# Kernel tuning notes

Measured on AMD Instinct MI355X. Metric: run time of the kernel, lower is better.

The kernel has to match this reference:

```python
import jax, jax.numpy as jnp
import numpy as np

BZ, PZ, FZ, FI = 8, 8192, 768, 256


def setup_inputs() -> dict:
    key = jax.random.key(0)
    ks = jax.random.split(key, 8)
    x = jax.random.normal(ks[0], (BZ, PZ, FZ), dtype=jnp.float32)
    # valid lengths per bag, in [1, PZ]
    nonpad = jax.random.randint(ks[1], (BZ,), 1, PZ + 1, dtype=jnp.int64)
    s_v = 1.0 / np.sqrt(FZ)
    V_w = jax.random.uniform(ks[2], (FI, FZ), minval=-s_v, maxval=s_v, dtype=jnp.float32)
    V_b = jax.random.uniform(ks[3], (FI,), minval=-s_v, maxval=s_v, dtype=jnp.float32)
    U_w = jax.random.uniform(ks[4], (FI, FZ), minval=-s_v, maxval=s_v, dtype=jnp.float32)
    U_b = jax.random.uniform(ks[5], (FI,), minval=-s_v, maxval=s_v, dtype=jnp.float32)
    s_w = 1.0 / np.sqrt(FI)
    w_w = jax.random.uniform(ks[6], (1, FI), minval=-s_w, maxval=s_w, dtype=jnp.float32)
    w_b = jax.random.uniform(ks[7], (1,), minval=-s_w, maxval=s_w, dtype=jnp.float32)
    return {"x": x, "nonpad": nonpad, "V_w": V_w, "V_b": V_b, "U_w": U_w, "U_b": U_b, "w_w": w_w, "w_b": w_b}


def reference(x, nonpad, V_w, V_b, U_w, U_b, w_w, w_b):
    # gated attention branches: [b, p, fi]
    att_v = jnp.tanh(jnp.einsum("bpf,if->bpi", x, V_w) + V_b)
    att_u = jax.nn.sigmoid(jnp.einsum("bpf,if->bpi", x, U_w) + U_b)
    # attention logits: [b, p]
    att = jnp.einsum("bpi,oi->bpo", att_u * att_v, w_w)[..., 0] + w_b[0]
    # per-sample masked softmax over first nonpad[b] positions, zeros on pad
    mask = jnp.arange(PZ)[None, :] < nonpad[:, None]  # [b, p]
    neg_inf = jnp.finfo(att.dtype).min
    weight = jax.nn.softmax(jnp.where(mask, att, neg_inf), axis=1)
    weight = jnp.where(mask, weight, 0.0)
    return weight[:, None, :]  # [b, 1, p]
```

## Files before the change

### kernel.cpp

```cpp
#include <hip/hip_runtime.h>
#include <hip/hip_bf16.h>
#include <cmath>

#define BZ 8
#define PZ 8192
#define FZ 768
#define FI 256
#define M_TOTAL (BZ * PZ)
#define BM 128
#define BK 64
#define NKT (FZ / BK)
#define NB_TILE (128 * BK)

typedef __bf16 bf16_t;
typedef __bf16 bf16x8 __attribute__((ext_vector_type(8)));
typedef float f32x4 __attribute__((ext_vector_type(4)));

#define AS1 __attribute__((address_space(1)))
#define AS3 __attribute__((address_space(3)))

__global__ void pack_weights(const float* __restrict__ Vw,
                             const float* __restrict__ Uw,
                             bf16_t* __restrict__ Wc) {
    int pr = blockIdx.x;
    int j = pr >> 5, u = (pr >> 4) & 1, r = pr & 15;
    const float* src = (u ? Uw : Vw) + (size_t)(j * 16 + r) * FZ;
    int nb = pr >> 7, prl = pr & 127;
    for (int k = threadIdx.x; k < FZ; k += blockDim.x) {
        int t = k >> 6, slot = (k >> 3) & 7, jj = k & 7;
        Wc[(size_t)(nb * NKT + t) * NB_TILE + prl * 64 + ((slot ^ (prl & 7)) * 8 + jj)]
            = (bf16_t)src[k];
    }
}

__global__ __launch_bounds__(256, 3)
void gemm_gate(const float* __restrict__ x, const bf16_t* __restrict__ Wc,
               const float* __restrict__ Vb, const float* __restrict__ Ub,
               const float* __restrict__ ww, float* __restrict__ part) {
    __shared__ bf16_t As[BM * BK] __attribute__((aligned(16)));
    __shared__ bf16_t Bs[2][128 * BK] __attribute__((aligned(16)));

    const int bid = blockIdx.x;
    const int nb = (bid >> 3) & 3;
    const int mt = (bid & 7) | ((bid >> 5) << 3);
    const int tid = threadIdx.x;
    const int l = tid & 63, wv = tid >> 6;
    const int wm = wv >> 1, wn = wv & 1;
    const int row0 = mt * BM;

    f32x4 acc[4][4] = {};
    float4 abuf[8];
    const bf16_t* WcB = Wc + (size_t)nb * NKT * NB_TILE;

    auto issueA = [&](int t) {
        #pragma unroll
        for (int i = 0; i < 4; ++i) {
            int sidx = tid + i * 256;
            int row = sidx >> 3, sl = sidx & 7;
            const float* gp = x + (size_t)(row0 + row) * FZ + t * BK + sl * 8;
            abuf[2 * i]     = *(const float4*)gp;
            abuf[2 * i + 1] = *(const float4*)(gp + 4);
        }
    };
    auto writeA = [&]() {
        #pragma unroll
        for (int i = 0; i < 4; ++i) {
            int sidx = tid + i * 256;
            int row = sidx >> 3, sl = sidx & 7;
            float4 f0 = abuf[2 * i], f1 = abuf[2 * i + 1];
            bf16x8 v;
            v[0] = (bf16_t)f0.x; v[1] = (bf16_t)f0.y; v[2] = (bf16_t)f0.z; v[3] = (bf16_t)f0.w;
            v[4] = (bf16_t)f1.x; v[5] = (bf16_t)f1.y; v[6] = (bf16_t)f1.z; v[7] = (bf16_t)f1.w;
            *(bf16x8*)&As[row * 64 + (sl ^ (row & 7)) * 8] = v;
        }
    };
    auto issueB = [&](int t, int buf) {
        const bf16_t* src = WcB + (size_t)t * NB_TILE + wv * 2048 + l * 8;
        bf16_t* dst = &Bs[buf][wv * 2048];
        #pragma unroll
        for (int c = 0; c < 4; ++c)
            __builtin_amdgcn_global_load_lds(
                (const AS1 void*)(src + c * 512),
                (AS3 void*)(dst + c * 512), 16, 0, 0);
    };
    auto compute = [&](int buf) {
        #pragma unroll
        for (int kk = 0; kk < 2; ++kk) {
            int sg = kk * 4 + (l >> 4);
            bf16x8 af[4], bfr[4];
            #pragma unroll
            for (int fm = 0; fm < 4; ++fm) {
                int row = wm * 64 + fm * 16 + (l & 15);
                af[fm] = *(const bf16x8*)&As[row * 64 + ((sg ^ (row & 7)) * 8)];
            }
            #pragma unroll
            for (int fn = 0; fn < 4; ++fn) {
                int col = wn * 64 + fn * 16 + (l & 15);
                bfr[fn] = *(const bf16x8*)&Bs[buf][col * 64 + ((sg ^ (col & 7)) * 8)];
            }
            #pragma unroll
            for (int fm = 0; fm < 4; ++fm)
                #pragma unroll
                for (int fn = 0; fn < 4; ++fn)
                    acc[fm][fn] = __builtin_amdgcn_mfma_f32_16x16x32_bf16(
                        af[fm], bfr[fn], acc[fm][fn], 0, 0, 0);
        }
    };

    issueB(0, 0);
    asm volatile("" ::: "memory");
    issueA(0);
    asm volatile("" ::: "memory");
    writeA();
    asm volatile("s_waitcnt vmcnt(0) lgkmcnt(0)" ::: "memory");
    __builtin_amdgcn_s_barrier();

    #pragma unroll
    for (int t = 0; t < NKT; ++t) {
        const int cur = t & 1;
        if (t + 1 < NKT) {
            issueB(t + 1, cur ^ 1);
            asm volatile("" ::: "memory");
            issueA(t + 1);
            asm volatile("" ::: "memory");
        }
        compute(cur);
        if (t + 1 < NKT) {
            __builtin_amdgcn_s_barrier();
            writeA();
            asm volatile("s_waitcnt vmcnt(0) lgkmcnt(0)" ::: "memory");
            __builtin_amdgcn_s_barrier();
        }
    }

    const int c16 = l & 15;
    float vb[2], ub[2], wf[2];
    #pragma unroll
    for (int q = 0; q < 2; ++q) {
        int o = (nb * 4 + wn * 2 + q) * 16 + c16;
        vb[q] = Vb[o]; ub[q] = Ub[o]; wf[q] = ww[o];
    }
    const int slot = nb * 2 + wn;
    #pragma unroll
    for (int fm = 0; fm < 4; ++fm) {
        #pragma unroll
        for (int e = 0; e < 4; ++e) {
            float partial = 0.f;
            #pragma unroll
            for (int q = 0; q < 2; ++q) {
                float zv = acc[fm][2 * q][e] + vb[q];
                float zu = acc[fm][2 * q + 1][e] + ub[q];
                float th = 1.f - 2.f / (__expf(2.f * zv) + 1.f);
                float sg = 1.f / (1.f + __expf(-zu));
                partial += th * sg * wf[q];
            }
            partial += __shfl_xor(partial, 1);
            partial += __shfl_xor(partial, 2);
            partial += __shfl_xor(partial, 4);
            partial += __shfl_xor(partial, 8);
            if (c16 == 0) {
                int r = row0 + wm * 64 + fm * 16 + (l >> 4) * 4 + e;
                part[(size_t)slot * M_TOTAL + r] = partial;
            }
        }
    }
}

__global__ __launch_bounds__(1024)
void softmax_kernel(const float* __restrict__ part, const int* __restrict__ nonpad,
                    float* __restrict__ out) {
    __shared__ float satt[PZ];
    __shared__ float red[16];
    int b = blockIdx.x;
    int np = nonpad[b];
    int tid = threadIdx.x;

    for (int p = tid; p < PZ; p += 1024) {
        float s = 0.f;
        #pragma unroll
        for (int q = 0; q < 8; ++q) s += part[(size_t)q * M_TOTAL + b * PZ + p];
        satt[p] = s;
    }
    __syncthreads();

    float m = -3.4e38f;
    for (int p = tid; p < np; p += 1024) m = fmaxf(m, satt[p]);
    #pragma unroll
    for (int off = 32; off; off >>= 1) m = fmaxf(m, __shfl_xor(m, off));
    if ((tid & 63) == 0) red[tid >> 6] = m;
    __syncthreads();
    m = red[0];
    #pragma unroll
    for (int i = 1; i < 16; ++i) m = fmaxf(m, red[i]);
    __syncthreads();

    float sum = 0.f;
    for (int p = tid; p < np; p += 1024) sum += __expf(satt[p] - m);
    #pragma unroll
    for (int off = 32; off; off >>= 1) sum += __shfl_xor(sum, off);
    if ((tid & 63) == 0) red[tid >> 6] = sum;
    __syncthreads();
    float S = red[0];
    #pragma unroll
    for (int i = 1; i < 16; ++i) S += red[i];
    float inv = 1.f / S;

    for (int p = tid; p < PZ; p += 1024)
        out[b * PZ + p] = (p < np) ? __expf(satt[p] - m) * inv : 0.f;
}

extern "C" void kernel_launch(void* const* d_in, const int* in_sizes, int n_in,
                              void* d_out, int out_size, void* d_ws, size_t ws_size,
                              hipStream_t stream) {
    const float* x    = (const float*)d_in[0];
    const int* nonpad = (const int*)d_in[1];
    const float* V_w  = (const float*)d_in[2];
    const float* V_b  = (const float*)d_in[3];
    const float* U_w  = (const float*)d_in[4];
    const float* U_b  = (const float*)d_in[5];
    const float* w_w  = (const float*)d_in[6];

    bf16_t* Wc  = (bf16_t*)d_ws;
    float* part = (float*)((char*)d_ws + (size_t)512 * FZ * 2);
    float* out  = (float*)d_out;

    pack_weights<<<512, 128, 0, stream>>>(V_w, U_w, Wc);
    gemm_gate<<<2048, 256, 0, stream>>>(x, Wc, V_b, U_b, w_w, part);
    softmax_kernel<<<8, 1024, 0, stream>>>(part, nonpad, out);
}
```

Before: 94.03 us.

## Load A fragments directly from global into registers, bypassing LDS

Each wave now owns 32 rows and all 128 output columns. It loads its x rows straight from global memory into MFMA-layout registers and converts them to bf16 there, which removes the shared-memory A tile, the writeA stage and one barrier per k-step. Only B still goes through double-buffered LDS, and a partial vmcnt wait lets the next A prefetch stay in flight. The cost is that x loads become less coalesced (16 rows, 32-byte segments per lane group), and each B fragment is now reused across only 2 M-fragments. There are also fewer partial slots for the softmax to sum.

```diff
diff --git a/kernel.cpp b/kernel.cpp
--- a/kernel.cpp
+++ b/kernel.cpp
@@ -37,7 +37,6 @@
 void gemm_gate(const float* __restrict__ x, const bf16_t* __restrict__ Wc,
                const float* __restrict__ Vb, const float* __restrict__ Ub,
                const float* __restrict__ ww, float* __restrict__ part) {
-    __shared__ bf16_t As[BM * BK] __attribute__((aligned(16)));
     __shared__ bf16_t Bs[2][128 * BK] __attribute__((aligned(16)));
 
     const int bid = blockIdx.x;
@@ -45,34 +44,23 @@
     const int mt = (bid & 7) | ((bid >> 5) << 3);
     const int tid = threadIdx.x;
     const int l = tid & 63, wv = tid >> 6;
-    const int wm = wv >> 1, wn = wv & 1;
-    const int row0 = mt * BM;
-
-    f32x4 acc[4][4] = {};
+    const int row0 = mt * BM + wv * 32;
+    const int arow = row0 + (l & 15);
+    const float* xbase = x + (size_t)arow * FZ + (l >> 4) * 8;
+
+    f32x4 acc[2][8] = {};
     float4 abuf[8];
     const bf16_t* WcB = Wc + (size_t)nb * NKT * NB_TILE;
 
     auto issueA = [&](int t) {
         #pragma unroll
-        for (int i = 0; i < 4; ++i) {
-            int sidx = tid + i * 256;
-            int row = sidx >> 3, sl = sidx & 7;
-            const float* gp = x + (size_t)(row0 + row) * FZ + t * BK + sl * 8;
-            abuf[2 * i]     = *(const float4*)gp;
-            abuf[2 * i + 1] = *(const float4*)(gp + 4);
-        }
-    };
-    auto writeA = [&]() {
-        #pragma unroll
-        for (int i = 0; i < 4; ++i) {
-            int sidx = tid + i * 256;
-            int row = sidx >> 3, sl = sidx & 7;
-            float4 f0 = abuf[2 * i], f1 = abuf[2 * i + 1];
-            bf16x8 v;
-            v[0] = (bf16_t)f0.x; v[1] = (bf16_t)f0.y; v[2] = (bf16_t)f0.z; v[3] = (bf16_t)f0.w;
-            v[4] = (bf16_t)f1.x; v[5] = (bf16_t)f1.y; v[6] = (bf16_t)f1.z; v[7] = (bf16_t)f1.w;
-            *(bf16x8*)&As[row * 64 + (sl ^ (row & 7)) * 8] = v;
-        }
+        for (int fm = 0; fm < 2; ++fm)
+            #pragma unroll
+            for (int kk = 0; kk < 2; ++kk) {
+                const float* gp = xbase + (size_t)fm * 16 * FZ + t * BK + kk * 32;
+                abuf[fm * 4 + kk * 2]     = *(const float4*)gp;
+                abuf[fm * 4 + kk * 2 + 1] = *(const float4*)(gp + 4);
+            }
     };
     auto issueB = [&](int t, int buf) {
         const bf16_t* src = WcB + (size_t)t * NB_TILE + wv * 2048 + l * 8;
@@ -83,71 +71,67 @@
                 (const AS1 void*)(src + c * 512),
                 (AS3 void*)(dst + c * 512), 16, 0, 0);
     };
-    auto compute = [&](int buf) {
-        #pragma unroll
-        for (int kk = 0; kk < 2; ++kk) {
-            int sg = kk * 4 + (l >> 4);
-            bf16x8 af[4], bfr[4];
-            #pragma unroll
-            for (int fm = 0; fm < 4; ++fm) {
-                int row = wm * 64 + fm * 16 + (l & 15);
-                af[fm] = *(const bf16x8*)&As[row * 64 + ((sg ^ (row & 7)) * 8)];
-            }
-            #pragma unroll
-            for (int fn = 0; fn < 4; ++fn) {
-                int col = wn * 64 + fn * 16 + (l & 15);
-                bfr[fn] = *(const bf16x8*)&Bs[buf][col * 64 + ((sg ^ (col & 7)) * 8)];
-            }
-            #pragma unroll
-            for (int fm = 0; fm < 4; ++fm)
-                #pragma unroll
-                for (int fn = 0; fn < 4; ++fn)
-                    acc[fm][fn] = __builtin_amdgcn_mfma_f32_16x16x32_bf16(
-                        af[fm], bfr[fn], acc[fm][fn], 0, 0, 0);
-        }
-    };
 
     issueB(0, 0);
     asm volatile("" ::: "memory");
     issueA(0);
     asm volatile("" ::: "memory");
-    writeA();
-    asm volatile("s_waitcnt vmcnt(0) lgkmcnt(0)" ::: "memory");
+    asm volatile("s_waitcnt vmcnt(8)" ::: "memory");
     __builtin_amdgcn_s_barrier();
 
     #pragma unroll
     for (int t = 0; t < NKT; ++t) {
         const int cur = t & 1;
+        bf16x8 afr[4];
+        #pragma unroll
+        for (int fm = 0; fm < 2; ++fm)
+            #pragma unroll
+            for (int kk = 0; kk < 2; ++kk) {
+                float4 f0 = abuf[fm * 4 + kk * 2], f1 = abuf[fm * 4 + kk * 2 + 1];
+                bf16x8 v;
+                v[0] = (bf16_t)f0.x; v[1] = (bf16_t)f0.y; v[2] = (bf16_t)f0.z; v[3] = (bf16_t)f0.w;
+                v[4] = (bf16_t)f1.x; v[5] = (bf16_t)f1.y; v[6] = (bf16_t)f1.z; v[7] = (bf16_t)f1.w;
+                afr[fm * 2 + kk] = v;
+            }
         if (t + 1 < NKT) {
             issueB(t + 1, cur ^ 1);
             asm volatile("" ::: "memory");
             issueA(t + 1);
             asm volatile("" ::: "memory");
         }
-        compute(cur);
+        #pragma unroll
+        for (int kk = 0; kk < 2; ++kk) {
+            int sg = kk * 4 + (l >> 4);
+            #pragma unroll
+            for (int fn = 0; fn < 8; ++fn) {
+                int col = fn * 16 + (l & 15);
+                bf16x8 bfr = *(const bf16x8*)&Bs[cur][col * 64 + ((sg ^ (col & 7)) * 8)];
+                #pragma unroll
+                for (int fm = 0; fm < 2; ++fm)
+                    acc[fm][fn] = __builtin_amdgcn_mfma_f32_16x16x32_bf16(
+                        afr[fm * 2 + kk], bfr, acc[fm][fn], 0, 0, 0);
+            }
+        }
         if (t + 1 < NKT) {
+            asm volatile("s_waitcnt vmcnt(8)" ::: "memory");
             __builtin_amdgcn_s_barrier();
-            writeA();
-            asm volatile("s_waitcnt vmcnt(0) lgkmcnt(0)" ::: "memory");
-            __builtin_amdgcn_s_barrier();
         }
     }
 
     const int c16 = l & 15;
-    float vb[2], ub[2], wf[2];
-    #pragma unroll
-    for (int q = 0; q < 2; ++q) {
-        int o = (nb * 4 + wn * 2 + q) * 16 + c16;
+    float vb[4], ub[4], wf[4];
+    #pragma unroll
+    for (int q = 0; q < 4; ++q) {
+        int o = (nb * 4 + q) * 16 + c16;
         vb[q] = Vb[o]; ub[q] = Ub[o]; wf[q] = ww[o];
     }
-    const int slot = nb * 2 + wn;
-    #pragma unroll
-    for (int fm = 0; fm < 4; ++fm) {
+    #pragma unroll
+    for (int fm = 0; fm < 2; ++fm) {
         #pragma unroll
         for (int e = 0; e < 4; ++e) {
             float partial = 0.f;
             #pragma unroll
-            for (int q = 0; q < 2; ++q) {
+            for (int q = 0; q < 4; ++q) {
                 float zv = acc[fm][2 * q][e] + vb[q];
                 float zu = acc[fm][2 * q + 1][e] + ub[q];
                 float th = 1.f - 2.f / (__expf(2.f * zv) + 1.f);
@@ -159,8 +143,8 @@
             partial += __shfl_xor(partial, 4);
             partial += __shfl_xor(partial, 8);
             if (c16 == 0) {
-                int r = row0 + wm * 64 + fm * 16 + (l >> 4) * 4 + e;
-                part[(size_t)slot * M_TOTAL + r] = partial;
+                int r = row0 + fm * 16 + (l >> 4) * 4 + e;
+                part[(size_t)nb * M_TOTAL + r] = partial;
             }
         }
     }
@@ -178,7 +162,7 @@
     for (int p = tid; p < PZ; p += 1024) {
         float s = 0.f;
         #pragma unroll
-        for (int q = 0; q < 8; ++q) s += part[(size_t)q * M_TOTAL + b * PZ + p];
+        for (int q = 0; q < 4; ++q) s += part[(size_t)q * M_TOTAL + b * PZ + p];
         satt[p] = s;
     }
     __syncthreads();
```

Measured after the change: 123.2 us. 31.0% more time.
